# Performance work log

Measured on AMD Instinct MI355X. Metric: run time of the kernel, lower is better.

Reference implementation:

```python
import jax, jax.numpy as jnp
import numpy as np

DIM = 512
WS = 7            # window size
N = WS * WS       # tokens per window
H = 16            # num heads
HD = DIM // H     # head dim
SCALE = HD ** -0.5
B_ = 2048         # batch * num_windows
NW = 64           # windows per image (mask leading dim)


def _relative_position_index():
    coords = np.stack(np.meshgrid(np.arange(WS), np.arange(WS), indexing='ij'))  # [2,WS,WS]
    cf = coords.reshape(2, -1)
    rel = cf[:, :, None] - cf[:, None, :]           # [2,N,N]
    rel = rel.transpose(1, 2, 0)
    rel[:, :, 0] += WS - 1
    rel[:, :, 1] += WS - 1
    rel[:, :, 0] *= 2 * WS - 1
    return rel.sum(-1).astype(np.int32)             # [N,N]

REL_IDX = _relative_position_index()


def setup_inputs() -> dict:
    key = jax.random.key(0)
    ks = jax.random.split(key, 7)
    return {
        'x': jax.random.normal(ks[0], (B_, N, DIM), jnp.float32),
        'mask': jax.random.normal(ks[1], (NW, N, N), jnp.float32),
        'qkv_w': jax.random.normal(ks[2], (DIM, 3 * DIM), jnp.float32) * 0.02,
        'qkv_b': jax.random.normal(ks[3], (3 * DIM,), jnp.float32) * 0.02,
        'proj_w': jax.random.normal(ks[4], (DIM, DIM), jnp.float32) * 0.02,
        'proj_b': jax.random.normal(ks[5], (DIM,), jnp.float32) * 0.02,
        'bias_table': jax.random.normal(ks[6], (169, H), jnp.float32) * 0.02,
    }


def reference(x, mask, qkv_w, qkv_b, proj_w, proj_b, bias_table):
    B, n, c = x.shape
    qkv = x @ qkv_w + qkv_b                              # [B,N,3C]
    qkv = qkv.reshape(B, n, 3, H, HD).transpose(2, 0, 3, 1, 4)  # [3,B,H,N,hd]
    q, k, v = qkv[0], qkv[1], qkv[2]
    attn = jnp.einsum('bhid,bhjd->bhij', q * SCALE, k)   # [B,H,N,N]
    # relative position bias gather: [N*N,H] -> [H,N,N]
    rel_bias = bias_table[REL_IDX.reshape(-1)].reshape(n, n, H).transpose(2, 0, 1)
    attn = attn + rel_bias[None]
    # shifted-window mask add: [B//nW, nW, H, N, N]
    attn = attn.reshape(B // NW, NW, H, n, n) + mask[None, :, None]
    attn = attn.reshape(B, H, n, n)
    attn = jax.nn.softmax(attn, axis=-1)
    out = jnp.einsum('bhij,bhjd->bhid', attn, v)         # [B,H,N,hd]
    out = out.transpose(0, 2, 1, 3).reshape(B, n, c)
    return out @ proj_w + proj_b
```

## Files before the change

### kernel.cpp

```cpp
#include <hip/hip_runtime.h>
#include <cstdint>

#define NTOK  49
#define NHEAD 16
#define HD    32
#define BATCH 2048
#define MTOT  (BATCH*NTOK)
#define SCALE 0.17677669529663687f

typedef float  f32x4  __attribute__((ext_vector_type(4)));
typedef __bf16 bf16x8 __attribute__((ext_vector_type(8)));
typedef unsigned int u32;
typedef const u32 __attribute__((address_space(1)))* gas_u32p;
typedef u32 __attribute__((address_space(3)))* las_u32p;

__device__ __forceinline__ void gld16(__bf16* lds, const __bf16* g) {
    __builtin_amdgcn_global_load_lds((gas_u32p)(const void*)g, (las_u32p)(void*)lds, 16, 0, 0);
}


__global__ __launch_bounds__(256) void cvt_x(const float* __restrict__ x,
                                             __bf16* __restrict__ o, long n) {
    long i = ((long)blockIdx.x * 256 + threadIdx.x) * 8;
    if (i >= n) return;
    float4 a = *(const float4*)(x + i);
    float4 b = *(const float4*)(x + i + 4);
    bf16x8 t;
    t[0] = (__bf16)a.x; t[1] = (__bf16)a.y; t[2] = (__bf16)a.z; t[3] = (__bf16)a.w;
    t[4] = (__bf16)b.x; t[5] = (__bf16)b.y; t[6] = (__bf16)b.z; t[7] = (__bf16)b.w;
    *(bf16x8*)(o + i) = t;
}

__global__ __launch_bounds__(256) void prep_w(const float* __restrict__ qkv_w,
                                              const float* __restrict__ proj_w,
                                              const float* __restrict__ qkv_b,
                                              __bf16* __restrict__ wqkv_t,
                                              __bf16* __restrict__ wp_t,
                                              float* __restrict__ qkvb_s) {
    int idx = blockIdx.x * 256 + threadIdx.x;
    if (idx < 1536 * 512) {
        int nn = idx >> 9, kk = idx & 511;
        float v = qkv_w[kk * 1536 + nn];
        if (nn < 512) v *= SCALE;
        wqkv_t[idx] = (__bf16)v;
    } else if (idx < 1536 * 512 + 512 * 512) {
        int j = idx - 1536 * 512;
        int nn = j >> 9, kk = j & 511;
        wp_t[j] = (__bf16)proj_w[kk * 512 + nn];
    } else if (idx < 1536 * 512 + 512 * 512 + 1536) {
        int n = idx - (1536 * 512 + 512 * 512);
        float v = qkv_b[n];
        if (n < 512) v *= SCALE;
        qkvb_s[n] = v;
    }
}

__global__ __launch_bounds__(256) void prep_addm(const float* __restrict__ mask,
                                                 const float* __restrict__ bias_table,
                                                 float* __restrict__ addm) {
    int idx = blockIdx.x * 256 + threadIdx.x;
    int i = idx & 63, j = (idx >> 6) & 63, w = (idx >> 12) & 63, h = idx >> 18;
    float v;
    if (j >= 49)      v = -1e30f;
    else if (i >= 49) v = 0.f;
    else {
        int ai = (i * 37) >> 8, aj = i - ai * 7;
        int bi = (j * 37) >> 8, bj = j - bi * 7;
        int ridx = (ai - bi + 6) * 13 + (aj - bj + 6);
        v = bias_table[ridx * 16 + h] + mask[(w * 49 + i) * 49 + j];
    }
    addm[idx] = v;
}


template <int OUT_BF16>
__global__ __launch_bounds__(256)
void gemm_k512(const __bf16* __restrict__ A, const __bf16* __restrict__ Bt,
               const float* __restrict__ bias, void* __restrict__ Cout, int N) {
    __shared__ __bf16 a_sh[128 * 32];
    __shared__ __bf16 b_sh[128 * 32];
    const int tid = threadIdx.x;
    const int wid = tid >> 6;
    const int lane = tid & 63;
    const int g = lane >> 4, c = lane & 15;
    const int r = lane >> 2;
    const int c8 = (lane & 3) * 8;
    const long m0 = (long)blockIdx.y * 128;
    const long n0 = (long)blockIdx.x * 128;

    const __bf16* aA = A + (m0 + wid * 32 + r) * 512 + c8;
    const __bf16* aB = Bt + (n0 + wid * 32 + r) * 512 + c8;
    __bf16* lA = a_sh + wid * 32 * 32;
    __bf16* lB = b_sh + wid * 32 * 32;

    f32x4 acc[4][4];
    for (int i = 0; i < 4; ++i)
        for (int j = 0; j < 4; ++j) acc[i][j] = (f32x4){0.f, 0.f, 0.f, 0.f};

    const int wm = (wid >> 1) * 64;
    const int wn = (wid & 1) * 64;

    for (int kt = 0; kt < 16; ++kt) {
        const int ko = kt * 32;
        gld16(lA,           aA + ko);
        gld16(lA + 16 * 32, aA + (long)16 * 512 + ko);
        gld16(lB,           aB + ko);
        gld16(lB + 16 * 32, aB + (long)16 * 512 + ko);
        __syncthreads();
        bf16x8 af[4], bf[4];
        for (int mt = 0; mt < 4; ++mt)
            af[mt] = *(const bf16x8*)(a_sh + (wm + mt * 16 + c) * 32 + g * 8);
        for (int nt = 0; nt < 4; ++nt)
            bf[nt] = *(const bf16x8*)(b_sh + (wn + nt * 16 + c) * 32 + g * 8);
        for (int mt = 0; mt < 4; ++mt)
            for (int nt = 0; nt < 4; ++nt)
                acc[mt][nt] = __builtin_amdgcn_mfma_f32_16x16x32_bf16(af[mt], bf[nt], acc[mt][nt], 0, 0, 0);
        __syncthreads();
    }

    for (int nt = 0; nt < 4; ++nt) {
        const long n = n0 + wn + nt * 16 + c;
        const float bv = bias[n];
        for (int mt = 0; mt < 4; ++mt) {
            const long row0 = m0 + wm + mt * 16 + g * 4;
            for (int rr = 0; rr < 4; ++rr) {
                float v = acc[mt][nt][rr] + bv;
                if (OUT_BF16) ((__bf16*)Cout)[(row0 + rr) * (long)N + n] = (__bf16)v;
                else          ((float*)Cout)[(row0 + rr) * (long)N + n] = v;
            }
        }
    }
}


__global__ __launch_bounds__(256)
void attn_k(const __bf16* __restrict__ qkv, const float* __restrict__ addm,
            __bf16* __restrict__ ao) {
    __shared__ float p_all[4][64 * 68];
    const int tid = threadIdx.x;
    const int wid = tid >> 6;
    const int lane = tid & 63;
    const int g = lane >> 4, c = lane & 15;
    const int wv = blockIdx.x * 4 + wid;
    const int b = wv >> 4, h = wv & 15;
    const int w = b & 63;
    float* psh = p_all[wid];

    const __bf16* base = qkv + (long)b * 49 * 1536;

    bf16x8 zero8;
    for (int i = 0; i < 8; ++i) zero8[i] = (__bf16)0.f;

    bf16x8 aq[4], bk[4];
    for (int t4 = 0; t4 < 4; ++t4) {
        int t = t4 * 16 + c;
        const __bf16* p = base + (long)t * 1536 + h * 32 + g * 8;
        bool ok = t < 49;
        aq[t4] = ok ? *(const bf16x8*)p : zero8;
        bk[t4] = ok ? *(const bf16x8*)(p + 512) : zero8;
    }

    const float* am = addm + (long)(h * 64 + w) * 64 * 64;
    f32x4 acc[4][4];
    for (int mt = 0; mt < 4; ++mt)
        for (int nt = 0; nt < 4; ++nt) {
            const float4 v = *(const float4*)(am + (long)(nt * 16 + c) * 64 + mt * 16 + g * 4);
            acc[mt][nt] = (f32x4){v.x, v.y, v.z, v.w};
        }

    for (int mt = 0; mt < 4; ++mt)
        for (int nt = 0; nt < 4; ++nt)
            acc[mt][nt] = __builtin_amdgcn_mfma_f32_16x16x32_bf16(aq[mt], bk[nt], acc[mt][nt], 0, 0, 0);

    float linv[4][4];
    for (int mt = 0; mt < 4; ++mt)
        for (int rr = 0; rr < 4; ++rr) {
            float mx = fmaxf(fmaxf(acc[mt][0][rr], acc[mt][1][rr]),
                             fmaxf(acc[mt][2][rr], acc[mt][3][rr]));
            for (int s = 1; s < 16; s <<= 1) mx = fmaxf(mx, __shfl_xor(mx, s));
            float sum = 0.f;
            for (int nt = 0; nt < 4; ++nt) {
                float p = __expf(acc[mt][nt][rr] - mx);
                acc[mt][nt][rr] = p;
                sum += p;
            }
            for (int s = 1; s < 16; s <<= 1) sum += __shfl_xor(sum, s);
            linv[mt][rr] = 1.0f / sum;
        }

    for (int mt = 0; mt < 4; ++mt)
        for (int nt = 0; nt < 4; ++nt)
            for (int rr = 0; rr < 4; ++rr)
                psh[(mt * 16 + g * 4 + rr) * 68 + nt * 16 + c] = acc[mt][nt][rr];
    __syncthreads();

    bf16x8 bv[2][2];
    const __bf16* vbase = base + 1024 + h * 32;
    for (int nt = 0; nt < 2; ++nt)
        for (int k2 = 0; k2 < 2; ++k2) {
            bf16x8 t = zero8;
            int d = nt * 16 + c;
            for (int jj = 0; jj < 8; ++jj) {
                int tok = k2 * 32 + g * 8 + jj;
                if (tok < 49) t[jj] = vbase[(long)tok * 1536 + d];
            }
            bv[nt][k2] = t;
        }

    bf16x8 ap[4][2];
    for (int mt = 0; mt < 4; ++mt)
        for (int k2 = 0; k2 < 2; ++k2) {
            const float* pp = psh + (mt * 16 + c) * 68 + k2 * 32 + g * 8;
            float4 x0 = *(const float4*)pp;
            float4 x1 = *(const float4*)(pp + 4);
            bf16x8 t;
            t[0] = (__bf16)x0.x; t[1] = (__bf16)x0.y; t[2] = (__bf16)x0.z; t[3] = (__bf16)x0.w;
            t[4] = (__bf16)x1.x; t[5] = (__bf16)x1.y; t[6] = (__bf16)x1.z; t[7] = (__bf16)x1.w;
            ap[mt][k2] = t;
        }

    f32x4 oacc[4][2];
    for (int mt = 0; mt < 4; ++mt)
        for (int nt = 0; nt < 2; ++nt) oacc[mt][nt] = (f32x4){0.f, 0.f, 0.f, 0.f};
    for (int mt = 0; mt < 4; ++mt)
        for (int nt = 0; nt < 2; ++nt)
            for (int k2 = 0; k2 < 2; ++k2)
                oacc[mt][nt] = __builtin_amdgcn_mfma_f32_16x16x32_bf16(ap[mt][k2], bv[nt][k2], oacc[mt][nt], 0, 0, 0);

    __bf16* obase = ao + (long)b * 49 * 512 + h * 32;
    for (int mt = 0; mt < 4; ++mt)
        for (int rr = 0; rr < 4; ++rr) {
            int i = mt * 16 + g * 4 + rr;
            if (i < 49) {
                float s = linv[mt][rr];
                for (int nt = 0; nt < 2; ++nt)
                    obase[(long)i * 512 + nt * 16 + c] = (__bf16)(oacc[mt][nt][rr] * s);
            }
        }
}


extern "C" void kernel_launch(void* const* d_in, const int* in_sizes, int n_in,
                              void* d_out, int out_size, void* d_ws, size_t ws_size,
                              hipStream_t stream) {
    const float* x      = (const float*)d_in[0];
    const float* mask   = (const float*)d_in[1];
    const float* qkv_w  = (const float*)d_in[2];
    const float* qkv_b  = (const float*)d_in[3];
    const float* proj_w = (const float*)d_in[4];
    const float* proj_b = (const float*)d_in[5];
    const float* btab   = (const float*)d_in[6];
    float* out = (float*)d_out;

    char* ws = (char*)d_ws;
    __bf16* ws_x   = (__bf16*)ws;
    __bf16* ws_ao  = (__bf16*)ws;
    __bf16* ws_qkv = (__bf16*)(ws + 102760448L);
    __bf16* wqkv_t = (__bf16*)(ws + 411041792L);
    __bf16* wp_t   = (__bf16*)(ws + 412614656L);
    float*  qkvb_s = (float*)(ws + 413138944L);
    float*  addm   = (float*)(ws + 413145088L);

    const long XN = (long)MTOT * 512;

    cvt_x<<<25088, 256, 0, stream>>>(x, ws_x, XN);
    prep_w<<<4102, 256, 0, stream>>>(qkv_w, proj_w, qkv_b, wqkv_t, wp_t, qkvb_s);
    prep_addm<<<16384, 256, 0, stream>>>(mask, btab, addm);

    gemm_k512<1><<<dim3(12, 784), 256, 0, stream>>>(ws_x, wqkv_t, qkvb_s, (void*)ws_qkv, 1536);
    attn_k<<<8192, 256, 0, stream>>>(ws_qkv, addm, ws_ao);
    gemm_k512<0><<<dim3(4, 784), 256, 0, stream>>>(ws_ao, wp_t, proj_b, (void*)out, 512);
}
```

Before: 989.8 us.

## Store V transposed per head and keep softmax probs in bf16 LDS

The QKV GEMM epilogue now splits its output into a Q/K buffer and a per-(window, head) transposed V buffer padded to 64 tokens. This lets the attention kernel load V with vector loads instead of strided scalar gathers. The attention kernel writes normalized probabilities as bf16 to LDS and computes O^T = V^T·P^T, which allows 4-wide vector output stores. The mask/bias table is also pre-laid out in MFMA fragment order so each lane does contiguous f32x4 loads. The cost moves to scattered 2-byte stores in the GEMM epilogue for the V part, and the per-warp __syncthreads before the LDS reads was removed, which appears safe because each warp only touches its own LDS region.

```diff
diff --git a/kernel.cpp b/kernel.cpp
--- a/kernel.cpp
+++ b/kernel.cpp
@@ -10,6 +10,7 @@
 
 typedef float  f32x4  __attribute__((ext_vector_type(4)));
 typedef __bf16 bf16x8 __attribute__((ext_vector_type(8)));
+typedef __bf16 bf16x4 __attribute__((ext_vector_type(4)));
 typedef unsigned int u32;
 typedef const u32 __attribute__((address_space(1)))* gas_u32p;
 typedef u32 __attribute__((address_space(3)))* las_u32p;
@@ -59,7 +60,15 @@
                                                  const float* __restrict__ bias_table,
                                                  float* __restrict__ addm) {
     int idx = blockIdx.x * 256 + threadIdx.x;
-    int i = idx & 63, j = (idx >> 6) & 63, w = (idx >> 12) & 63, h = idx >> 18;
+    int rr   = idx & 3;
+    int lane = (idx >> 2) & 63;
+    int tile = (idx >> 8) & 15;
+    int w    = (idx >> 12) & 63;
+    int h    = idx >> 18;
+    int mt = tile >> 2, nt = tile & 3;
+    int g = lane >> 4, c = lane & 15;
+    int i = mt * 16 + g * 4 + rr;
+    int j = nt * 16 + c;
     float v;
     if (j >= 49)      v = -1e30f;
     else if (i >= 49) v = 0.f;
@@ -73,10 +82,11 @@
 }
 
 
-template <int OUT_BF16>
+template <int MODE>
 __global__ __launch_bounds__(256)
 void gemm_k512(const __bf16* __restrict__ A, const __bf16* __restrict__ Bt,
-               const float* __restrict__ bias, void* __restrict__ Cout, int N) {
+               const float* __restrict__ bias, float* __restrict__ outF,
+               __bf16* __restrict__ outQK, __bf16* __restrict__ outVT, int N) {
     __shared__ __bf16 a_sh[128 * 32];
     __shared__ __bf16 b_sh[128 * 32];
     const int tid = threadIdx.x;
@@ -123,10 +133,21 @@
         const float bv = bias[n];
         for (int mt = 0; mt < 4; ++mt) {
             const long row0 = m0 + wm + mt * 16 + g * 4;
-            for (int rr = 0; rr < 4; ++rr) {
-                float v = acc[mt][nt][rr] + bv;
-                if (OUT_BF16) ((__bf16*)Cout)[(row0 + rr) * (long)N + n] = (__bf16)v;
-                else          ((float*)Cout)[(row0 + rr) * (long)N + n] = v;
+            if (MODE == 0) {
+                for (int rr = 0; rr < 4; ++rr)
+                    outF[(row0 + rr) * (long)N + n] = acc[mt][nt][rr] + bv;
+            } else if (n0 < 1024) {
+                for (int rr = 0; rr < 4; ++rr)
+                    outQK[(row0 + rr) * 1024 + n] = (__bf16)(acc[mt][nt][rr] + bv);
+            } else {
+                const int h = ((int)n - 1024) >> 5;
+                const int d = ((int)n - 1024) & 31;
+                for (int rr = 0; rr < 4; ++rr) {
+                    int row = (int)row0 + rr;
+                    int b2 = row / 49;
+                    int t2 = row - b2 * 49;
+                    outVT[(long)(b2 * 512 + h * 32 + d) * 64 + t2] = (__bf16)(acc[mt][nt][rr] + bv);
+                }
             }
         }
     }
@@ -134,9 +155,9 @@
 
 
 __global__ __launch_bounds__(256)
-void attn_k(const __bf16* __restrict__ qkv, const float* __restrict__ addm,
-            __bf16* __restrict__ ao) {
-    __shared__ float p_all[4][64 * 68];
+void attn_k(const __bf16* __restrict__ qk, const __bf16* __restrict__ vT,
+            const float* __restrict__ addm, __bf16* __restrict__ ao) {
+    __shared__ __bf16 p_all[4][64 * 72];
     const int tid = threadIdx.x;
     const int wid = tid >> 6;
     const int lane = tid & 63;
@@ -144,9 +165,9 @@
     const int wv = blockIdx.x * 4 + wid;
     const int b = wv >> 4, h = wv & 15;
     const int w = b & 63;
-    float* psh = p_all[wid];
-
-    const __bf16* base = qkv + (long)b * 49 * 1536;
+    __bf16* psh = p_all[wid];
+
+    const __bf16* base = qk + (long)b * 49 * 1024 + h * 32;
 
     bf16x8 zero8;
     for (int i = 0; i < 8; ++i) zero8[i] = (__bf16)0.f;
@@ -154,19 +175,17 @@
     bf16x8 aq[4], bk[4];
     for (int t4 = 0; t4 < 4; ++t4) {
         int t = t4 * 16 + c;
-        const __bf16* p = base + (long)t * 1536 + h * 32 + g * 8;
+        const __bf16* p = base + (long)t * 1024 + g * 8;
         bool ok = t < 49;
         aq[t4] = ok ? *(const bf16x8*)p : zero8;
         bk[t4] = ok ? *(const bf16x8*)(p + 512) : zero8;
     }
 
-    const float* am = addm + (long)(h * 64 + w) * 64 * 64;
+    const float* am = addm + (long)(h * 64 + w) * 4096;
     f32x4 acc[4][4];
     for (int mt = 0; mt < 4; ++mt)
-        for (int nt = 0; nt < 4; ++nt) {
-            const float4 v = *(const float4*)(am + (long)(nt * 16 + c) * 64 + mt * 16 + g * 4);
-            acc[mt][nt] = (f32x4){v.x, v.y, v.z, v.w};
-        }
+        for (int nt = 0; nt < 4; ++nt)
+            acc[mt][nt] = *(const f32x4*)(am + (mt * 4 + nt) * 256 + lane * 4);
 
     for (int mt = 0; mt < 4; ++mt)
         for (int nt = 0; nt < 4; ++nt)
@@ -191,52 +210,42 @@
     for (int mt = 0; mt < 4; ++mt)
         for (int nt = 0; nt < 4; ++nt)
             for (int rr = 0; rr < 4; ++rr)
-                psh[(mt * 16 + g * 4 + rr) * 68 + nt * 16 + c] = acc[mt][nt][rr];
-    __syncthreads();
-
-    bf16x8 bv[2][2];
-    const __bf16* vbase = base + 1024 + h * 32;
-    for (int nt = 0; nt < 2; ++nt)
-        for (int k2 = 0; k2 < 2; ++k2) {
-            bf16x8 t = zero8;
-            int d = nt * 16 + c;
-            for (int jj = 0; jj < 8; ++jj) {
-                int tok = k2 * 32 + g * 8 + jj;
-                if (tok < 49) t[jj] = vbase[(long)tok * 1536 + d];
-            }
-            bv[nt][k2] = t;
-        }
-
-    bf16x8 ap[4][2];
-    for (int mt = 0; mt < 4; ++mt)
-        for (int k2 = 0; k2 < 2; ++k2) {
-            const float* pp = psh + (mt * 16 + c) * 68 + k2 * 32 + g * 8;
-            float4 x0 = *(const float4*)pp;
-            float4 x1 = *(const float4*)(pp + 4);
-            bf16x8 t;
-            t[0] = (__bf16)x0.x; t[1] = (__bf16)x0.y; t[2] = (__bf16)x0.z; t[3] = (__bf16)x0.w;
-            t[4] = (__bf16)x1.x; t[5] = (__bf16)x1.y; t[6] = (__bf16)x1.z; t[7] = (__bf16)x1.w;
-            ap[mt][k2] = t;
-        }
-
-    f32x4 oacc[4][2];
-    for (int mt = 0; mt < 4; ++mt)
-        for (int nt = 0; nt < 2; ++nt) oacc[mt][nt] = (f32x4){0.f, 0.f, 0.f, 0.f};
-    for (int mt = 0; mt < 4; ++mt)
-        for (int nt = 0; nt < 2; ++nt)
+                psh[(mt * 16 + g * 4 + rr) * 72 + nt * 16 + c] =
+                    (__bf16)(acc[mt][nt][rr] * linv[mt][rr]);
+
+    const __bf16* vb = vT + (long)(b * 16 + h) * 2048;
+    bf16x8 av[2][2];
+    for (int mt2 = 0; mt2 < 2; ++mt2)
+        for (int k2 = 0; k2 < 2; ++k2)
+            av[mt2][k2] = *(const bf16x8*)(vb + (mt2 * 16 + c) * 64 + k2 * 32 + g * 8);
+
+    bf16x8 bp[4][2];
+    for (int nt2 = 0; nt2 < 4; ++nt2)
+        for (int k2 = 0; k2 < 2; ++k2)
+            bp[nt2][k2] = *(const bf16x8*)(psh + (nt2 * 16 + c) * 72 + k2 * 32 + g * 8);
+
+    f32x4 oacc[2][4];
+    for (int mt2 = 0; mt2 < 2; ++mt2)
+        for (int nt2 = 0; nt2 < 4; ++nt2) oacc[mt2][nt2] = (f32x4){0.f, 0.f, 0.f, 0.f};
+    for (int mt2 = 0; mt2 < 2; ++mt2)
+        for (int nt2 = 0; nt2 < 4; ++nt2)
             for (int k2 = 0; k2 < 2; ++k2)
-                oacc[mt][nt] = __builtin_amdgcn_mfma_f32_16x16x32_bf16(ap[mt][k2], bv[nt][k2], oacc[mt][nt], 0, 0, 0);
+                oacc[mt2][nt2] = __builtin_amdgcn_mfma_f32_16x16x32_bf16(av[mt2][k2], bp[nt2][k2], oacc[mt2][nt2], 0, 0, 0);
 
     __bf16* obase = ao + (long)b * 49 * 512 + h * 32;
-    for (int mt = 0; mt < 4; ++mt)
-        for (int rr = 0; rr < 4; ++rr) {
-            int i = mt * 16 + g * 4 + rr;
-            if (i < 49) {
-                float s = linv[mt][rr];
-                for (int nt = 0; nt < 2; ++nt)
-                    obase[(long)i * 512 + nt * 16 + c] = (__bf16)(oacc[mt][nt][rr] * s);
+    for (int nt2 = 0; nt2 < 4; ++nt2) {
+        int i = nt2 * 16 + c;
+        if (i < 49) {
+            for (int mt2 = 0; mt2 < 2; ++mt2) {
+                bf16x4 t;
+                t[0] = (__bf16)oacc[mt2][nt2][0];
+                t[1] = (__bf16)oacc[mt2][nt2][1];
+                t[2] = (__bf16)oacc[mt2][nt2][2];
+                t[3] = (__bf16)oacc[mt2][nt2][3];
+                *(bf16x4*)(obase + (long)i * 512 + mt2 * 16 + g * 4) = t;
             }
         }
+    }
 }
 
 
@@ -255,11 +264,12 @@
     char* ws = (char*)d_ws;
     __bf16* ws_x   = (__bf16*)ws;
     __bf16* ws_ao  = (__bf16*)ws;
-    __bf16* ws_qkv = (__bf16*)(ws + 102760448L);
-    __bf16* wqkv_t = (__bf16*)(ws + 411041792L);
-    __bf16* wp_t   = (__bf16*)(ws + 412614656L);
-    float*  qkvb_s = (float*)(ws + 413138944L);
-    float*  addm   = (float*)(ws + 413145088L);
+    __bf16* ws_qk  = (__bf16*)(ws + 102760448L);
+    __bf16* wqkv_t = (__bf16*)(ws + 308281344L);
+    __bf16* wp_t   = (__bf16*)(ws + 309854208L);
+    float*  qkvb_s = (float*)(ws + 310378496L);
+    float*  addm   = (float*)(ws + 310384640L);
+    __bf16* ws_vT  = (__bf16*)(ws + 327161856L);
 
     const long XN = (long)MTOT * 512;
 
@@ -267,7 +277,7 @@
     prep_w<<<4102, 256, 0, stream>>>(qkv_w, proj_w, qkv_b, wqkv_t, wp_t, qkvb_s);
     prep_addm<<<16384, 256, 0, stream>>>(mask, btab, addm);
 
-    gemm_k512<1><<<dim3(12, 784), 256, 0, stream>>>(ws_x, wqkv_t, qkvb_s, (void*)ws_qkv, 1536);
-    attn_k<<<8192, 256, 0, stream>>>(ws_qkv, addm, ws_ao);
-    gemm_k512<0><<<dim3(4, 784), 256, 0, stream>>>(ws_ao, wp_t, proj_b, (void*)out, 512);
-}
+    gemm_k512<1><<<dim3(12, 784), 256, 0, stream>>>(ws_x, wqkv_t, qkvb_s, nullptr, ws_qk, ws_vT, 1536);
+    attn_k<<<8192, 256, 0, stream>>>(ws_qk, ws_vT, addm, ws_ao);
+    gemm_k512<0><<<dim3(4, 784), 256, 0, stream>>>(ws_ao, wp_t, proj_b, out, nullptr, nullptr, 512);
+}
```

After: 965.7 us. -2.4%, faster.
